# Optimization experiments

Measured on AMD Instinct MI355X. Metric: run time of the kernel, lower is better.

The kernel has to match this reference:

```python
import jax, jax.numpy as jnp
import numpy as np

N_BINS = 10  # matches init_kwargs n_bins

def setup_inputs() -> dict:
    key = jax.random.key(0)
    k1, k2 = jax.random.split(key)
    N, C = 262144, 128
    logits = jax.random.normal(k1, (N, C), dtype=jnp.float32)
    targets = jax.random.randint(k2, (N,), 0, C, dtype=jnp.int64)
    return {"logits": logits, "targets": targets}

def reference(logits, targets):
    # probs / confidence / prediction
    probs = jax.nn.softmax(logits, axis=1)                 # [N, C]
    confidences = jnp.max(probs, axis=1)                   # [N]
    predictions = jnp.argmax(probs, axis=1)                # [N]
    accuracies = (predictions == targets).astype(logits.dtype)

    # bin id for (lower, upper] bins of width 1/N_BINS:
    # conf in (k/N_BINS, (k+1)/N_BINS]  ->  ceil(conf*N_BINS)-1 == k
    bin_ids = jnp.clip(
        jnp.ceil(confidences * N_BINS).astype(jnp.int32) - 1, 0, N_BINS - 1
    )

    n = confidences.shape[0]
    ones = jnp.ones_like(confidences)
    counts = jax.ops.segment_sum(ones, bin_ids, num_segments=N_BINS)        # [B]
    sum_conf = jax.ops.segment_sum(confidences, bin_ids, num_segments=N_BINS)
    sum_acc = jax.ops.segment_sum(accuracies, bin_ids, num_segments=N_BINS)

    safe_counts = jnp.maximum(counts, 1.0)
    avg_conf = sum_conf / safe_counts
    avg_acc = sum_acc / safe_counts
    prop_in_bin = counts / n
    per_bin = jnp.where(counts > 0, jnp.abs(avg_conf - avg_acc) * prop_in_bin, 0.0)
    return jnp.sum(per_bin)
```

## Files before the change

kernel.cpp:

```cpp
#include <hip/hip_runtime.h>
#include <hip/hip_bf16.h>

#define NBINS 10
#define C 128
#define U 8
#define NREP 64
#define REPSTRIDE 32


__global__ __launch_bounds__(256) void ece_main_kernel(
    const float* __restrict__ logits, const int* __restrict__ targets,
    unsigned long long* __restrict__ gbins, int N) {
  __shared__ unsigned long long sbins[3 * NBINS];
  const int tid = threadIdx.x;
  for (int i = tid; i < 3 * NBINS; i += blockDim.x) sbins[i] = 0ull;
  __syncthreads();

  const int lane = tid & 63;
  const int half = lane >> 5;
  const int hl = lane & 31;
  const int wavesPerBlock = blockDim.x >> 6;
  const int wid = blockIdx.x * wavesPerBlock + (tid >> 6);
  const int nwaves = gridDim.x * wavesPerBlock;

  const int npairs = N >> 1;

  for (int p0 = wid * U; p0 < npairs; p0 += nwaves * U) {
    float4 v[U];
    int tg[U];
    const bool full = (p0 + U) <= npairs;

    if (full) {
      const float* base = logits + ((size_t)p0 * 2 + half) * C + (hl << 2);
      #pragma unroll
      for (int u = 0; u < U; ++u)
        v[u] = *reinterpret_cast<const float4*>(base + u * (2 * C));
      if (hl == 0) {
        const int* tb = targets + p0 * 2 + half;
        #pragma unroll
        for (int u = 0; u < U; ++u) tg[u] = tb[2 * u];
      }
    } else {
      #pragma unroll
      for (int u = 0; u < U; ++u) {
        const int p = p0 + u;
        const int pc = p < npairs ? p : npairs - 1;
        v[u] = *reinterpret_cast<const float4*>(
            logits + (size_t)pc * (2 * C) + half * C + (hl << 2));
      }
      if (hl == 0) {
        #pragma unroll
        for (int u = 0; u < U; ++u) {
          const int p = p0 + u;
          const int pc = p < npairs ? p : npairs - 1;
          tg[u] = targets[pc * 2 + half];
        }
      }
    }

    float s[U];
    #pragma unroll
    for (int u = 0; u < U; ++u)
      s[u] = (__expf(v[u].x) + __expf(v[u].y)) +
             (__expf(v[u].z) + __expf(v[u].w));

    float m[U], lm[U];
    int col[U];
    #pragma unroll
    for (int u = 0; u < U; ++u) {
      float mm = v[u].x; int c = 0;
      if (v[u].y > mm) { mm = v[u].y; c = 1; }
      if (v[u].z > mm) { mm = v[u].z; c = 2; }
      if (v[u].w > mm) { mm = v[u].w; c = 3; }
      m[u] = mm; lm[u] = mm; col[u] = (hl << 2) + c;
    }

    #pragma unroll
    for (int off = 1; off <= 16; off <<= 1) {
      #pragma unroll
      for (int u = 0; u < U; ++u) m[u] = fmaxf(m[u], __shfl_xor(m[u], off));
      #pragma unroll
      for (int u = 0; u < U; ++u) s[u] += __shfl_xor(s[u], off);
    }

    int wcol[U];
    #pragma unroll
    for (int u = 0; u < U; ++u) {
      const unsigned long long b = __ballot(lm[u] == m[u]);
      const unsigned slice = (unsigned)(b >> (half << 5));
      const int srcl = (half << 5) + (__ffs(slice) - 1);
      wcol[u] = __shfl(col[u], srcl);
    }

    if (hl == 0) {
      #pragma unroll
      for (int u = 0; u < U; ++u) {
        if (full || (p0 + u) < npairs) {
          const float conf = __expf(m[u]) / s[u];
          int bin = (int)ceilf(conf * 10.0f) - 1;
          bin = min(max(bin, 0), NBINS - 1);
          const unsigned long long acc = (tg[u] == wcol[u]) ? 1ull : 0ull;
          const unsigned long long confq =
              (unsigned long long)((double)conf * 4294967296.0);
          atomicAdd(&sbins[bin], 1ull);
          atomicAdd(&sbins[NBINS + bin], confq);
          atomicAdd(&sbins[2 * NBINS + bin], acc);
        }
      }
    }
  }

  if ((N & 1) && wid == 0 && half == 0) {
    const int row = N - 1;
    const float4 x = *reinterpret_cast<const float4*>(
        logits + (size_t)row * C + (hl << 2));
    float m = x.x; int c = 0;
    if (x.y > m) { m = x.y; c = 1; }
    if (x.z > m) { m = x.z; c = 2; }
    if (x.w > m) { m = x.w; c = 3; }
    const float lmv = m;
    const int col = (hl << 2) + c;
    float s = (__expf(x.x) + __expf(x.y)) + (__expf(x.z) + __expf(x.w));
    #pragma unroll
    for (int off = 1; off <= 16; off <<= 1) {
      m = fmaxf(m, __shfl_xor(m, off));
      s += __shfl_xor(s, off);
    }
    const unsigned long long b = __ballot(lmv == m);
    const int srcl = __ffs((unsigned)b) - 1;
    const int wcol = __shfl(col, srcl);
    if (hl == 0) {
      const float conf = __expf(m) / s;
      int bin = (int)ceilf(conf * 10.0f) - 1;
      bin = min(max(bin, 0), NBINS - 1);
      const unsigned long long acc = (targets[row] == wcol) ? 1ull : 0ull;
      const unsigned long long confq =
          (unsigned long long)((double)conf * 4294967296.0);
      atomicAdd(&sbins[bin], 1ull);
      atomicAdd(&sbins[NBINS + bin], confq);
      atomicAdd(&sbins[2 * NBINS + bin], acc);
    }
  }

  __syncthreads();
  unsigned long long* rep =
      gbins + (size_t)(blockIdx.x & (NREP - 1)) * REPSTRIDE;
  for (int i = tid; i < 3 * NBINS; i += blockDim.x) {
    unsigned long long vv = sbins[i];
    if (vv) atomicAdd(&rep[i], vv);
  }
}

__global__ void ece_final_kernel(const unsigned long long* __restrict__ gbins,
                                 float* __restrict__ out, int N) {
  __shared__ unsigned long long tot[3 * NBINS];
  const int t = threadIdx.x;
  if (t < 3 * NBINS) {
    unsigned long long s = 0ull;
    #pragma unroll 8
    for (int r = 0; r < NREP; ++r) s += gbins[(size_t)r * REPSTRIDE + t];
    tot[t] = s;
  }
  __syncthreads();
  float per = 0.0f;
  if (t < NBINS) {
    const double cnt = (double)tot[t];
    const double sc = (double)tot[NBINS + t] * (1.0 / 4294967296.0);
    const double sa = (double)tot[2 * NBINS + t];
    const double safe = cnt > 0.0 ? cnt : 1.0;
    const double avg_c = sc / safe;
    const double avg_a = sa / safe;
    const double prop = cnt / (double)N;
    per = (cnt > 0.0) ? (float)(fabs(avg_c - avg_a) * prop) : 0.0f;
  }
  #pragma unroll
  for (int off = 1; off < 16; off <<= 1) per += __shfl_xor(per, off);
  if (t == 0) out[0] = per;
}

extern "C" void kernel_launch(void* const* d_in, const int* in_sizes, int n_in,
                              void* d_out, int out_size, void* d_ws, size_t ws_size,
                              hipStream_t stream) {
  const float* logits = (const float*)d_in[0];
  const int* targets = (const int*)d_in[1];
  float* out = (float*)d_out;
  unsigned long long* gbins = (unsigned long long*)d_ws;

  const int N = in_sizes[1];

  hipMemsetAsync(gbins, 0, NREP * REPSTRIDE * sizeof(unsigned long long),
                 stream);

  const int block = 256;
  const int wavesPerBlock = block / 64;
  const int npairs = N >> 1;
  int grid = (npairs + wavesPerBlock * U - 1) / (wavesPerBlock * U);
  if (grid < 1) grid = 1;

  ece_main_kernel<<<grid, block, 0, stream>>>(logits, targets, gbins, N);
  ece_final_kernel<<<1, 64, 0, stream>>>(gbins, out, N);
}
```

Before: 39.44 us.

## Use DPP row reductions and target-logit compare instead of argmax ballot

Replaces the shuffle-xor butterfly reductions for max and sum with DPP row_shr/row_bcast steps, so the result lands in lane 16 of each half-wave, and moves the bin-update work to that lane. Accuracy is now computed by reading the target's logit and comparing it to the row max, which removes the per-lane column tracking, ballot and extra shuffle. Count and accuracy are packed into one 32-bit LDS atomic, cutting three 64-bit atomics to two. Ties in the max now count as correct for any tied column, unlike argmax's first index, and the packed 16-bit fields could overflow if one block put more than 65535 rows in a bin.

```diff
diff --git a/kernel.cpp b/kernel.cpp
--- a/kernel.cpp
+++ b/kernel.cpp
@@ -8,12 +8,31 @@
 #define REPSTRIDE 32
 
 
+template <int CTRL, int RMASK>
+__device__ __forceinline__ void red_step(float (&m)[U], float (&s)[U]) {
+  #pragma unroll
+  for (int u = 0; u < U; ++u) {
+    const float tm = __int_as_float(__builtin_amdgcn_update_dpp(
+        (int)0xFF800000 ,
+        __float_as_int(m[u]), CTRL, RMASK, 0xF, true));
+    m[u] = fmaxf(m[u], tm);
+  }
+  #pragma unroll
+  for (int u = 0; u < U; ++u) {
+    const float ts = __int_as_float(__builtin_amdgcn_update_dpp(
+        0 ,
+        __float_as_int(s[u]), CTRL, RMASK, 0xF, true));
+    s[u] += ts;
+  }
+}
+
 __global__ __launch_bounds__(256) void ece_main_kernel(
     const float* __restrict__ logits, const int* __restrict__ targets,
     unsigned long long* __restrict__ gbins, int N) {
-  __shared__ unsigned long long sbins[3 * NBINS];
+  __shared__ unsigned scount[NBINS];
+  __shared__ unsigned long long sconf[NBINS];
   const int tid = threadIdx.x;
-  for (int i = tid; i < 3 * NBINS; i += blockDim.x) sbins[i] = 0ull;
+  if (tid < NBINS) { scount[tid] = 0u; sconf[tid] = 0ull; }
   __syncthreads();
 
   const int lane = tid & 63;
@@ -29,13 +48,14 @@
     float4 v[U];
     int tg[U];
     const bool full = (p0 + U) <= npairs;
+    const float* rowbase = logits + ((size_t)p0 * 2 + half) * C;
 
     if (full) {
-      const float* base = logits + ((size_t)p0 * 2 + half) * C + (hl << 2);
+      const float* base = rowbase + (hl << 2);
       #pragma unroll
       for (int u = 0; u < U; ++u)
         v[u] = *reinterpret_cast<const float4*>(base + u * (2 * C));
-      if (hl == 0) {
+      if (hl == 16) {
         const int* tb = targets + p0 * 2 + half;
         #pragma unroll
         for (int u = 0; u < U; ++u) tg[u] = tb[2 * u];
@@ -48,7 +68,7 @@
         v[u] = *reinterpret_cast<const float4*>(
             logits + (size_t)pc * (2 * C) + half * C + (hl << 2));
       }
-      if (hl == 0) {
+      if (hl == 16) {
         #pragma unroll
         for (int u = 0; u < U; ++u) {
           const int p = p0 + u;
@@ -64,47 +84,30 @@
       s[u] = (__expf(v[u].x) + __expf(v[u].y)) +
              (__expf(v[u].z) + __expf(v[u].w));
 
-    float m[U], lm[U];
-    int col[U];
+    float m[U];
     #pragma unroll
-    for (int u = 0; u < U; ++u) {
-      float mm = v[u].x; int c = 0;
-      if (v[u].y > mm) { mm = v[u].y; c = 1; }
-      if (v[u].z > mm) { mm = v[u].z; c = 2; }
-      if (v[u].w > mm) { mm = v[u].w; c = 3; }
-      m[u] = mm; lm[u] = mm; col[u] = (hl << 2) + c;
-    }
-
-    #pragma unroll
-    for (int off = 1; off <= 16; off <<= 1) {
-      #pragma unroll
-      for (int u = 0; u < U; ++u) m[u] = fmaxf(m[u], __shfl_xor(m[u], off));
-      #pragma unroll
-      for (int u = 0; u < U; ++u) s[u] += __shfl_xor(s[u], off);
-    }
-
-    int wcol[U];
-    #pragma unroll
-    for (int u = 0; u < U; ++u) {
-      const unsigned long long b = __ballot(lm[u] == m[u]);
-      const unsigned slice = (unsigned)(b >> (half << 5));
-      const int srcl = (half << 5) + (__ffs(slice) - 1);
-      wcol[u] = __shfl(col[u], srcl);
-    }
-
-    if (hl == 0) {
+    for (int u = 0; u < U; ++u)
+      m[u] = fmaxf(fmaxf(v[u].x, v[u].y), fmaxf(v[u].z, v[u].w));
+
+    red_step<0x121, 0xF>(m, s);
+    red_step<0x122, 0xF>(m, s);
+    red_step<0x124, 0xF>(m, s);
+    red_step<0x128, 0xF>(m, s);
+    red_step<0x142, 0xA>(m, s);
+
+    if (hl == 16) {
       #pragma unroll
       for (int u = 0; u < U; ++u) {
         if (full || (p0 + u) < npairs) {
+          const float xt = rowbase[(size_t)u * (2 * C) + tg[u]];
+          const unsigned acc = (xt == m[u]) ? 1u : 0u;
           const float conf = __expf(m[u]) / s[u];
           int bin = (int)ceilf(conf * 10.0f) - 1;
           bin = min(max(bin, 0), NBINS - 1);
-          const unsigned long long acc = (tg[u] == wcol[u]) ? 1ull : 0ull;
           const unsigned long long confq =
               (unsigned long long)((double)conf * 4294967296.0);
-          atomicAdd(&sbins[bin], 1ull);
-          atomicAdd(&sbins[NBINS + bin], confq);
-          atomicAdd(&sbins[2 * NBINS + bin], acc);
+          atomicAdd(&scount[bin], 0x10000u + acc);
+          atomicAdd(&sconf[bin], confq);
         }
       }
     }
@@ -114,40 +117,36 @@
     const int row = N - 1;
     const float4 x = *reinterpret_cast<const float4*>(
         logits + (size_t)row * C + (hl << 2));
-    float m = x.x; int c = 0;
-    if (x.y > m) { m = x.y; c = 1; }
-    if (x.z > m) { m = x.z; c = 2; }
-    if (x.w > m) { m = x.w; c = 3; }
-    const float lmv = m;
-    const int col = (hl << 2) + c;
+    float m = fmaxf(fmaxf(x.x, x.y), fmaxf(x.z, x.w));
     float s = (__expf(x.x) + __expf(x.y)) + (__expf(x.z) + __expf(x.w));
     #pragma unroll
     for (int off = 1; off <= 16; off <<= 1) {
       m = fmaxf(m, __shfl_xor(m, off));
       s += __shfl_xor(s, off);
     }
-    const unsigned long long b = __ballot(lmv == m);
-    const int srcl = __ffs((unsigned)b) - 1;
-    const int wcol = __shfl(col, srcl);
     if (hl == 0) {
+      const float xt = logits[(size_t)row * C + targets[row]];
+      const unsigned acc = (xt == m) ? 1u : 0u;
       const float conf = __expf(m) / s;
       int bin = (int)ceilf(conf * 10.0f) - 1;
       bin = min(max(bin, 0), NBINS - 1);
-      const unsigned long long acc = (targets[row] == wcol) ? 1ull : 0ull;
       const unsigned long long confq =
           (unsigned long long)((double)conf * 4294967296.0);
-      atomicAdd(&sbins[bin], 1ull);
-      atomicAdd(&sbins[NBINS + bin], confq);
-      atomicAdd(&sbins[2 * NBINS + bin], acc);
+      atomicAdd(&scount[bin], 0x10000u + acc);
+      atomicAdd(&sconf[bin], confq);
     }
   }
 
   __syncthreads();
   unsigned long long* rep =
       gbins + (size_t)(blockIdx.x & (NREP - 1)) * REPSTRIDE;
-  for (int i = tid; i < 3 * NBINS; i += blockDim.x) {
-    unsigned long long vv = sbins[i];
-    if (vv) atomicAdd(&rep[i], vv);
+  if (tid < NBINS) {
+    const unsigned pc = scount[tid];
+    if (pc) {
+      atomicAdd(&rep[tid], (unsigned long long)(pc >> 16));
+      atomicAdd(&rep[NBINS + tid], sconf[tid]);
+      atomicAdd(&rep[2 * NBINS + tid], (unsigned long long)(pc & 0xFFFFu));
+    }
   }
 }
 
```

After: 41.28 us. 1.05x slower.
